# Optimization experiments

Hardware: AMD Instinct MI355X
Metric: run time of the kernel (lower is better)

## Reference

```python
import jax, jax.numpy as jnp
import numpy as np

BETA = 0.5
THR = 1.0
BN_EPS = 1e-5

@jax.custom_vjp
def spike(x):
    # heaviside fire: spk = 1[x > 0]
    return (x > 0).astype(x.dtype)

def _spike_fwd(x):
    return spike(x), x

def _spike_bwd(x, g):
    # snnTorch surrogate.atan(), alpha=2: grad = (alpha/2) / (1 + (pi/2*alpha*x)^2) = 1/(1+(pi*x)^2)
    return (g / (1.0 + (jnp.pi * x) ** 2),)

spike.defvjp(_spike_fwd, _spike_bwd)

def setup_inputs() -> dict:
    key = jax.random.key(0)
    ks = jax.random.split(key, 6)
    B, T, D, O = 512, 128, 512, 10
    data = jax.random.normal(ks[0], (B, T, D), dtype=jnp.float32)
    # deterministic Dropout(0.5) mask in {0, 2} (scaled by 1/keep_prob), time-major
    u = jax.random.uniform(ks[1], (T, B, D), dtype=jnp.float32)
    drop_mask = (u > 0.5).astype(jnp.float32) * 2.0
    W1 = jax.random.normal(ks[2], (D, D), dtype=jnp.float32) / np.sqrt(D)
    b1 = jax.random.normal(ks[3], (D,), dtype=jnp.float32) * 0.01
    gamma = jnp.ones((D,), dtype=jnp.float32)
    bn_beta = jnp.zeros((D,), dtype=jnp.float32)
    W2 = jax.random.normal(ks[4], (O, D), dtype=jnp.float32) / np.sqrt(D)
    b2 = jax.random.normal(ks[5], (O,), dtype=jnp.float32) * 0.01
    return {"data": data, "drop_mask": drop_mask, "W1": W1, "b1": b1,
            "gamma": gamma, "bn_beta": bn_beta, "W2": W2, "b2": b2}

def reference(data, drop_mask, W1, b1, gamma, bn_beta, W2, b2):
    B, T, D = data.shape
    O = W2.shape[0]
    xs = jnp.transpose(data, (1, 0, 2))  # [T, B, D] time-major

    def batchnorm(x):  # training-mode BatchNorm1d over batch dim
        mean = jnp.mean(x, axis=0)
        var = jnp.mean((x - mean) ** 2, axis=0)
        return gamma * (x - mean) * jax.lax.rsqrt(var + BN_EPS) + bn_beta

    def step(carry, inp):
        mem1, spk1, mem2, spk2 = carry
        xt, mt = inp
        cur1 = batchnorm((mt * xt) @ W1.T + b1)          # dropout -> linear -> BN
        mem1 = BETA * mem1 + cur1 - spk1 * THR           # Leaky, subtract reset
        spk1 = spike(mem1 - THR)
        cur2 = spk1 @ W2.T + b2
        mem2 = BETA * mem2 + cur2 - spk2 * THR
        spk2 = spike(mem2 - THR)
        return (mem1, spk1, mem2, spk2), spk2

    init = (jnp.zeros((B, D), data.dtype), jnp.zeros((B, D), data.dtype),
            jnp.zeros((B, O), data.dtype), jnp.zeros((B, O), data.dtype))
    _, spk_rec = jax.lax.scan(step, init, (xs, drop_mask))
    return spk_rec  # [T, B, out_size] == torch.stack(spk_rec)
```

## Files before the change

### kernel.cpp

```cpp
#include <hip/hip_runtime.h>
#include <math.h>

#define B_ 512
#define T_ 128
#define D_ 512
#define O_ 10

typedef unsigned int uint32;
typedef unsigned long long uint64;
typedef short bf16x8 __attribute__((ext_vector_type(8)));
typedef float f32x4 __attribute__((ext_vector_type(4)));

__device__ __forceinline__ uint32 bf16rne(float f) {
    uint32 u = __float_as_uint(f);
    return (u + 0x7FFFu + ((u >> 16) & 1u)) >> 16;
}
__device__ __forceinline__ float bf16f(uint32 h) { return __uint_as_float(h << 16); }

__global__ __launch_bounds__(256)
void presplitW_kernel(const float* __restrict__ W1, unsigned short* __restrict__ Wsp)
{
    const int idx = blockIdx.x * 256 + threadIdx.x;
    const float4 v = *(const float4*)(W1 + (size_t)idx * 4);
    float vv[4] = {v.x, v.y, v.z, v.w};
    uint32 c0[4], c1[4], c2[4];
#pragma unroll
    for (int i = 0; i < 4; ++i) {
        c0[i] = bf16rne(vv[i]);
        float r = vv[i] - bf16f(c0[i]);
        c1[i] = bf16rne(r);
        float r2 = r - bf16f(c1[i]);
        c2[i] = bf16rne(r2);
    }
    const size_t base = (size_t)idx * 4;
    uint2 w;
    w.x = c0[0] | (c0[1] << 16); w.y = c0[2] | (c0[3] << 16);
    *(uint2*)(Wsp + base) = w;
    w.x = c1[0] | (c1[1] << 16); w.y = c1[2] | (c1[3] << 16);
    *(uint2*)(Wsp + 262144 + base) = w;
    w.x = c2[0] | (c2[1] << 16); w.y = c2[2] | (c2[3] << 16);
    *(uint2*)(Wsp + 524288 + base) = w;
}

#define SPW 40
#define SPL (128*SPW)

__global__ __launch_bounds__(256)
void gemm1_kernel(const float* __restrict__ data, const float* __restrict__ drop,
                  const unsigned short* __restrict__ Wsp, const float* __restrict__ b1,
                  float* __restrict__ hbuf, double* __restrict__ pSum,
                  double* __restrict__ pSq, int t0, int Tc)
{
    __shared__ __align__(16) unsigned short As3[3 * SPL];
    __shared__ __align__(16) unsigned short Ws3[3 * SPL];

    const int tid = threadIdx.x;
    const int bid = blockIdx.x;
    const int xcd = bid & 7;
    const int rest = bid >> 3;
    const int yy = rest & 3;
    const int g = (rest >> 2) * 8 + xcd;

    const int R = g * 128;
    const int tc = R >> 9;
    const int b_base = R & 511;
    const int t = t0 + tc;
    const int d0 = yy * 128;

    const int w = tid >> 6;
    const int lane = tid & 63;
    const int wm = w & 1, wn = w >> 1;
    const int q = lane >> 4, r16 = lane & 15;

    f32x4 acc[4][4];
#pragma unroll
    for (int i = 0; i < 4; ++i)
#pragma unroll
        for (int j = 0; j < 4; ++j) acc[i][j] = (f32x4){0.f, 0.f, 0.f, 0.f};

    for (int k0 = 0; k0 < 512; k0 += 32) {
#pragma unroll
        for (int i = 0; i < 2; ++i) {
            const int p = tid + i * 256;
            const int m = p >> 2;
            const int kg = (p & 3) * 8;
            const float* dsrc = data + ((size_t)(b_base + m) * T_ + t) * D_ + k0 + kg;
            const float* msrc = drop + ((size_t)t * B_ + b_base + m) * D_ + k0 + kg;
            const float4 dv0 = *(const float4*)(dsrc);
            const float4 dv1 = *(const float4*)(dsrc + 4);
            const float4 mv0 = *(const float4*)(msrc);
            const float4 mv1 = *(const float4*)(msrc + 4);
            float vv[8] = {dv0.x*mv0.x, dv0.y*mv0.y, dv0.z*mv0.z, dv0.w*mv0.w,
                           dv1.x*mv1.x, dv1.y*mv1.y, dv1.z*mv1.z, dv1.w*mv1.w};
            uint32 u0[8], u1[8], u2[8];
#pragma unroll
            for (int e = 0; e < 8; ++e) {
                u0[e] = bf16rne(vv[e]);
                const float r = vv[e] - bf16f(u0[e]);
                u1[e] = bf16rne(r);
                const float r2 = r - bf16f(u1[e]);
                u2[e] = bf16rne(r2);
            }
            const int dst = m * SPW + kg;
            uint4 pk;
            pk.x = u0[0]|(u0[1]<<16); pk.y = u0[2]|(u0[3]<<16);
            pk.z = u0[4]|(u0[5]<<16); pk.w = u0[6]|(u0[7]<<16);
            *(uint4*)(&As3[dst]) = pk;
            pk.x = u1[0]|(u1[1]<<16); pk.y = u1[2]|(u1[3]<<16);
            pk.z = u1[4]|(u1[5]<<16); pk.w = u1[6]|(u1[7]<<16);
            *(uint4*)(&As3[SPL + dst]) = pk;
            pk.x = u2[0]|(u2[1]<<16); pk.y = u2[2]|(u2[3]<<16);
            pk.z = u2[4]|(u2[5]<<16); pk.w = u2[6]|(u2[7]<<16);
            *(uint4*)(&As3[2*SPL + dst]) = pk;
        }
#pragma unroll
        for (int i = 0; i < 6; ++i) {
            const int p = tid + i * 256;
            const int s = p >> 9;
            const int rem = p & 511;
            const int n = rem >> 2;
            const int kg = (rem & 3) * 8;
            const uint4 pk = *(const uint4*)(Wsp + (size_t)s * 262144
                                             + (size_t)(d0 + n) * 512 + k0 + kg);
            *(uint4*)(&Ws3[s * SPL + n * SPW + kg]) = pk;
        }
        __syncthreads();

        bf16x8 af[4][3], bfr[4][3];
#pragma unroll
        for (int mt = 0; mt < 4; ++mt)
#pragma unroll
            for (int s = 0; s < 3; ++s)
                af[mt][s] = *(const bf16x8*)(&As3[s*SPL + (wm*64 + mt*16 + r16)*SPW + q*8]);
#pragma unroll
        for (int nt = 0; nt < 4; ++nt)
#pragma unroll
            for (int s = 0; s < 3; ++s)
                bfr[nt][s] = *(const bf16x8*)(&Ws3[s*SPL + (wn*64 + nt*16 + r16)*SPW + q*8]);

#define PRODUCT(SA, SB)                                                          \
        {                                                                        \
            _Pragma("unroll")                                                    \
            for (int mt = 0; mt < 4; ++mt) {                                     \
                _Pragma("unroll")                                                \
                for (int nt = 0; nt < 4; ++nt)                                   \
                    acc[mt][nt] = __builtin_amdgcn_mfma_f32_16x16x32_bf16(       \
                        af[mt][SA], bfr[nt][SB], acc[mt][nt], 0, 0, 0);          \
            }                                                                    \
        }
        PRODUCT(0, 0)
        PRODUCT(0, 1)
        PRODUCT(1, 0)
        PRODUCT(1, 1)
        PRODUCT(0, 2)
        PRODUCT(2, 0)
#undef PRODUCT
        __syncthreads();
    }

    float b1c[4];
#pragma unroll
    for (int nt = 0; nt < 4; ++nt) b1c[nt] = b1[d0 + wn*64 + nt*16 + r16];

    double sd[4], sq[4];
#pragma unroll
    for (int nt = 0; nt < 4; ++nt) { sd[nt] = 0.0; sq[nt] = 0.0; }

#pragma unroll
    for (int mt = 0; mt < 4; ++mt)
#pragma unroll
        for (int r = 0; r < 4; ++r) {
            const int row = R + wm*64 + mt*16 + q*4 + r;
            float* op = hbuf + (size_t)row * D_ + d0 + wn*64 + r16;
#pragma unroll
            for (int nt = 0; nt < 4; ++nt) {
                const float hf = acc[mt][nt][r] + b1c[nt];
                op[nt*16] = hf;
                const double dh = (double)hf;
                sd[nt] += dh;
                sq[nt] = fma(dh, dh, sq[nt]);
            }
        }
#pragma unroll
    for (int nt = 0; nt < 4; ++nt) {
        sd[nt] += __shfl_xor(sd[nt], 16); sd[nt] += __shfl_xor(sd[nt], 32);
        sq[nt] += __shfl_xor(sq[nt], 16); sq[nt] += __shfl_xor(sq[nt], 32);
    }
    double* dsh = (double*)&As3[0];
    __syncthreads();
    if (q == 0) {
#pragma unroll
        for (int nt = 0; nt < 4; ++nt) {
            dsh[(w*64 + nt*16 + r16)*2 + 0] = sd[nt];
            dsh[(w*64 + nt*16 + r16)*2 + 1] = sq[nt];
        }
    }
    __syncthreads();
    if (tid < 128) {
        const int col = tid;
        const int gg = col >> 6, c = col & 63;
        const double S = dsh[((2*gg)*64 + c)*2 + 0] + dsh[((2*gg+1)*64 + c)*2 + 0];
        const double Q = dsh[((2*gg)*64 + c)*2 + 1] + dsh[((2*gg+1)*64 + c)*2 + 1];
        const int bt = b_base >> 7;
        pSum[((size_t)(bt*Tc + tc))*D_ + d0 + col] = S;
        pSq [((size_t)(bt*Tc + tc))*D_ + d0 + col] = Q;
    }
}

__global__ __launch_bounds__(256)
void finalize_kernel(const double* __restrict__ pSum, const double* __restrict__ pSq,
                     const float* __restrict__ gamma, const float* __restrict__ bn_beta,
                     float* __restrict__ scaleArr, float* __restrict__ shiftArr, int Tc)
{
    const int tc = blockIdx.x;
    const int d = blockIdx.y * 256 + threadIdx.x;
    double S = 0.0, Q = 0.0;
#pragma unroll
    for (int bt = 0; bt < 4; ++bt) {
        S += pSum[((size_t)(bt * Tc + tc)) * D_ + d];
        Q += pSq [((size_t)(bt * Tc + tc)) * D_ + d];
    }
    const double mean = S / (double)B_;
    const double var  = Q / (double)B_ - mean * mean;
    const double rs   = 1.0 / sqrt(var + 1e-5);
    const double gm   = (double)gamma[d] * rs;
    scaleArr[tc * D_ + d] = (float)gm;
    shiftArr[tc * D_ + d] = (float)((double)bn_beta[d] - gm * mean);
}

__global__ __launch_bounds__(256)
void scanA_kernel(const float* __restrict__ hbuf, const float* __restrict__ scaleArr,
                  const float* __restrict__ shiftArr, uint64* __restrict__ spkM,
                  float* __restrict__ sMem1, float* __restrict__ sSpk1, int t0, int Tc)
{
    const int e = blockIdx.x * 256 + threadIdx.x;
    const int b = e >> 9;
    const int d = e & 511;
    const int lane = threadIdx.x & 63;
    const int mword = (e >> 6);

    float m1, s1;
    if (t0 == 0) { m1 = 0.f; s1 = 0.f; }
    else { m1 = sMem1[e]; s1 = sSpk1[e]; }

    float hv = hbuf[e];
    float sc = scaleArr[d];
    float sf = shiftArr[d];

    for (int tc = 0; tc < Tc; ++tc) {
        float hvN, scN, sfN;
        if (tc + 1 < Tc) {
            hvN = hbuf[(size_t)(tc + 1) * (B_ * D_) + e];
            scN = scaleArr[(tc + 1) * D_ + d];
            sfN = shiftArr[(tc + 1) * D_ + d];
        }
        const float cur1 = fmaf(sc, hv, sf);
        m1 = fmaf(0.5f, m1, cur1) - s1;
        s1 = ((m1 - 1.0f) > 0.f) ? 1.f : 0.f;

        const uint64 mask = __ballot(s1 == 1.f);
        if (lane == 0)
            spkM[(size_t)tc * (B_ * 8) + mword] = mask;

        hv = hvN; sc = scN; sf = sfN;
    }

    sMem1[e] = m1;
    sSpk1[e] = s1;
}

__global__ __launch_bounds__(256)
void gemm2_kernel(const uint64* __restrict__ spkM, const float* __restrict__ W2,
                  const float* __restrict__ b2, float* __restrict__ cur2)
{
    const int tid = threadIdx.x;
    const int w = tid >> 6, lane = tid & 63;
    const int rowBase = blockIdx.x * 16 + w * 4;

    float w2r[O_][8];
#pragma unroll
    for (int o = 0; o < O_; ++o) {
        const float4 wa = *(const float4*)(W2 + o * D_ + lane * 8);
        const float4 wb = *(const float4*)(W2 + o * D_ + lane * 8 + 4);
        w2r[o][0] = wa.x; w2r[o][1] = wa.y; w2r[o][2] = wa.z; w2r[o][3] = wa.w;
        w2r[o][4] = wb.x; w2r[o][5] = wb.y; w2r[o][6] = wb.z; w2r[o][7] = wb.w;
    }
    float b2v[O_];
#pragma unroll
    for (int o = 0; o < O_; ++o) b2v[o] = b2[o];

    for (int rr = 0; rr < 4; ++rr) {
        const int row = rowBase + rr;
        const uint64 mk = spkM[(size_t)row * 8 + (lane >> 3)];
        const uint32 byte = (uint32)(mk >> ((lane & 7) * 8)) & 0xFFu;
        float f[8];
#pragma unroll
        for (int j = 0; j < 8; ++j)
            f[j] = (byte & (1u << j)) ? 1.0f : 0.0f;
        float p[O_];
#pragma unroll
        for (int o = 0; o < O_; ++o) {
            float v = f[0] * w2r[o][0];
#pragma unroll
            for (int j = 1; j < 8; ++j) v = fmaf(f[j], w2r[o][j], v);
            p[o] = v;
        }
#pragma unroll
        for (int o = 0; o < O_; ++o) {
#pragma unroll
            for (int off = 32; off > 0; off >>= 1)
                p[o] += __shfl_xor(p[o], off);
        }
        float outv = 0.f;
#pragma unroll
        for (int o = 0; o < O_; ++o)
            if (lane == o) outv = p[o] + b2v[o];
        if (lane < O_)
            cur2[(size_t)row * O_ + lane] = outv;
    }
}

__global__ __launch_bounds__(256)
void scanB_kernel(const float* __restrict__ cur2, float* __restrict__ out,
                  float* __restrict__ sMem2, float* __restrict__ sSpk2, int t0, int Tc)
{
    const int idx = blockIdx.x * 256 + threadIdx.x;
    float mem2, spk2;
    if (t0 == 0) { mem2 = 0.f; spk2 = 0.f; }
    else { mem2 = sMem2[idx]; spk2 = sSpk2[idx]; }

    float v[4], vn[4];
#pragma unroll
    for (int j = 0; j < 4; ++j) v[j] = cur2[(size_t)j * (B_ * O_) + idx];

    for (int tg = 0; tg < Tc; tg += 4) {
        if (tg + 4 < Tc) {
#pragma unroll
            for (int j = 0; j < 4; ++j)
                vn[j] = cur2[(size_t)(tg + 4 + j) * (B_ * O_) + idx];
        }
#pragma unroll
        for (int j = 0; j < 4; ++j) {
            mem2 = fmaf(0.5f, mem2, v[j]) - spk2;
            spk2 = ((mem2 - 1.0f) > 0.f) ? 1.f : 0.f;
            out[(size_t)(t0 + tg + j) * (B_ * O_) + idx] = spk2;
        }
#pragma unroll
        for (int j = 0; j < 4; ++j) v[j] = vn[j];
    }
    sMem2[idx] = mem2;
    sSpk2[idx] = spk2;
}

extern "C" void kernel_launch(void* const* d_in, const int* in_sizes, int n_in,
                              void* d_out, int out_size, void* d_ws, size_t ws_size,
                              hipStream_t stream) {
    const float* data    = (const float*)d_in[0];
    const float* drop    = (const float*)d_in[1];
    const float* W1      = (const float*)d_in[2];
    const float* b1      = (const float*)d_in[3];
    const float* gamma   = (const float*)d_in[4];
    const float* bn_beta = (const float*)d_in[5];
    const float* W2      = (const float*)d_in[6];
    const float* b2      = (const float*)d_in[7];
    float* out = (float*)d_out;

    const size_t fixedBytes = 1572864 + 2*1048576 + 2*20480;
    const size_t perT = 1048576 + 32768 + 20480 + 4096 + 32768;
    int Tc = T_;
    while (Tc > 2 && fixedBytes + (size_t)Tc * perT > ws_size) Tc >>= 1;

    char* p = (char*)d_ws;
    double* pSum    = (double*)p; p += (size_t)4 * Tc * D_ * 8;
    double* pSq     = (double*)p; p += (size_t)4 * Tc * D_ * 8;
    float* hbuf     = (float*)p; p += (size_t)Tc * B_ * D_ * 4;
    float* scaleArr = (float*)p; p += (size_t)Tc * D_ * 4;
    float* shiftArr = (float*)p; p += (size_t)Tc * D_ * 4;
    float* sMem1    = (float*)p; p += (size_t)B_ * D_ * 4;
    float* sSpk1    = (float*)p; p += (size_t)B_ * D_ * 4;
    float* sMem2    = (float*)p; p += (size_t)B_ * O_ * 4;
    float* sSpk2    = (float*)p; p += (size_t)B_ * O_ * 4;
    float* cur2     = (float*)p; p += (size_t)Tc * B_ * O_ * 4;
    unsigned short* Wsp = (unsigned short*)p; p += (size_t)3 * D_ * D_ * 2;
    uint64* spkM    = (uint64*)p; p += (size_t)Tc * B_ * 8 * 8;

    presplitW_kernel<<<256, 256, 0, stream>>>(W1, Wsp);

    for (int t0 = 0; t0 < T_; t0 += Tc) {
        gemm1_kernel<<<Tc * 16, 256, 0, stream>>>(data, drop, Wsp, b1, hbuf,
                                                  pSum, pSq, t0, Tc);
        finalize_kernel<<<dim3(Tc, D_ / 256), 256, 0, stream>>>(
            pSum, pSq, gamma, bn_beta, scaleArr, shiftArr, Tc);
        scanA_kernel<<<(B_ * D_) / 256, 256, 0, stream>>>(hbuf, scaleArr, shiftArr, spkM,
                                                          sMem1, sSpk1, t0, Tc);
        gemm2_kernel<<<Tc * 32, 256, 0, stream>>>(spkM, W2, b2, cur2);
        scanB_kernel<<<20, 256, 0, stream>>>(cur2, out, sMem2, sSpk2, t0, Tc);
    }
}
```

Measured before the change: 541.0 us.

## Fuse layer-1 scan, output projection and layer-2 scan into one kernel

Replaces the separate scanA, gemm2 and scanB kernels with one kernel that has a block per batch row. Each step, the block builds the spike mask in shared memory, projects it onto W2 and updates the layer-2 membrane in place. This drops the global spkM and cur2 buffers and two launches per chunk. In exchange it adds a __syncthreads per timestep, and every wave redundantly recomputes the full 10-output shuffle reduction for the row.

Measured after the change: 805.2 us. 1.49x slower.

```diff
diff --git a/kernel.cpp b/kernel.cpp
--- a/kernel.cpp
+++ b/kernel.cpp
@@ -228,54 +228,24 @@
     shiftArr[tc * D_ + d] = (float)((double)bn_beta[d] - gm * mean);
 }
 
-__global__ __launch_bounds__(256)
-void scanA_kernel(const float* __restrict__ hbuf, const float* __restrict__ scaleArr,
-                  const float* __restrict__ shiftArr, uint64* __restrict__ spkM,
-                  float* __restrict__ sMem1, float* __restrict__ sSpk1, int t0, int Tc)
+__global__ __launch_bounds__(512)
+void scan_fused_kernel(const float* __restrict__ hbuf, const float* __restrict__ scaleArr,
+                       const float* __restrict__ shiftArr, const float* __restrict__ W2,
+                       const float* __restrict__ b2, float* __restrict__ out,
+                       float* __restrict__ sMem1, float* __restrict__ sSpk1,
+                       float* __restrict__ sMem2, float* __restrict__ sSpk2,
+                       int t0, int Tc)
 {
-    const int e = blockIdx.x * 256 + threadIdx.x;
-    const int b = e >> 9;
-    const int d = e & 511;
-    const int lane = threadIdx.x & 63;
-    const int mword = (e >> 6);
+    const int b = blockIdx.x;
+    const int tid = threadIdx.x;
+    const int w = tid >> 6, lane = tid & 63;
+    const int e = b * D_ + tid;
+
+    __shared__ uint64 masks[2][8];
 
     float m1, s1;
     if (t0 == 0) { m1 = 0.f; s1 = 0.f; }
     else { m1 = sMem1[e]; s1 = sSpk1[e]; }
-
-    float hv = hbuf[e];
-    float sc = scaleArr[d];
-    float sf = shiftArr[d];
-
-    for (int tc = 0; tc < Tc; ++tc) {
-        float hvN, scN, sfN;
-        if (tc + 1 < Tc) {
-            hvN = hbuf[(size_t)(tc + 1) * (B_ * D_) + e];
-            scN = scaleArr[(tc + 1) * D_ + d];
-            sfN = shiftArr[(tc + 1) * D_ + d];
-        }
-        const float cur1 = fmaf(sc, hv, sf);
-        m1 = fmaf(0.5f, m1, cur1) - s1;
-        s1 = ((m1 - 1.0f) > 0.f) ? 1.f : 0.f;
-
-        const uint64 mask = __ballot(s1 == 1.f);
-        if (lane == 0)
-            spkM[(size_t)tc * (B_ * 8) + mword] = mask;
-
-        hv = hvN; sc = scN; sf = sfN;
-    }
-
-    sMem1[e] = m1;
-    sSpk1[e] = s1;
-}
-
-__global__ __launch_bounds__(256)
-void gemm2_kernel(const uint64* __restrict__ spkM, const float* __restrict__ W2,
-                  const float* __restrict__ b2, float* __restrict__ cur2)
-{
-    const int tid = threadIdx.x;
-    const int w = tid >> 6, lane = tid & 63;
-    const int rowBase = blockIdx.x * 16 + w * 4;
 
     float w2r[O_][8];
 #pragma unroll
@@ -289,9 +259,35 @@
 #pragma unroll
     for (int o = 0; o < O_; ++o) b2v[o] = b2[o];
 
-    for (int rr = 0; rr < 4; ++rr) {
-        const int row = rowBase + rr;
-        const uint64 mk = spkM[(size_t)row * 8 + (lane >> 3)];
+    float mem2, spk2;
+    if (t0 == 0) { mem2 = 0.f; spk2 = 0.f; }
+    else {
+        mem2 = (lane < O_) ? sMem2[b * O_ + lane] : 0.f;
+        spk2 = (lane < O_) ? sSpk2[b * O_ + lane] : 0.f;
+    }
+
+    float hv = hbuf[e];
+    float sc = scaleArr[tid];
+    float sf = shiftArr[tid];
+
+    for (int t = 0; t < Tc; ++t) {
+        float hvN, scN, sfN;
+        if (t + 1 < Tc) {
+            hvN = hbuf[(size_t)(t + 1) * (B_ * D_) + e];
+            scN = scaleArr[(t + 1) * D_ + tid];
+            sfN = shiftArr[(t + 1) * D_ + tid];
+        }
+
+        const float cur1 = fmaf(sc, hv, sf);
+        m1 = fmaf(0.5f, m1, cur1) - s1;
+        s1 = ((m1 - 1.0f) > 0.f) ? 1.f : 0.f;
+
+        const uint64 mask = __ballot(s1 == 1.f);
+        const int par = t & 1;
+        if (lane == 0) masks[par][w] = mask;
+        __syncthreads();
+
+        const uint64 mk = masks[par][lane >> 3];
         const uint32 byte = (uint32)(mk >> ((lane & 7) * 8)) & 0xFFu;
         float f[8];
 #pragma unroll
@@ -311,45 +307,27 @@
             for (int off = 32; off > 0; off >>= 1)
                 p[o] += __shfl_xor(p[o], off);
         }
-        float outv = 0.f;
+
+        float c2 = 0.f;
 #pragma unroll
         for (int o = 0; o < O_; ++o)
-            if (lane == o) outv = p[o] + b2v[o];
-        if (lane < O_)
-            cur2[(size_t)row * O_ + lane] = outv;
-    }
-}
-
-__global__ __launch_bounds__(256)
-void scanB_kernel(const float* __restrict__ cur2, float* __restrict__ out,
-                  float* __restrict__ sMem2, float* __restrict__ sSpk2, int t0, int Tc)
-{
-    const int idx = blockIdx.x * 256 + threadIdx.x;
-    float mem2, spk2;
-    if (t0 == 0) { mem2 = 0.f; spk2 = 0.f; }
-    else { mem2 = sMem2[idx]; spk2 = sSpk2[idx]; }
-
-    float v[4], vn[4];
-#pragma unroll
-    for (int j = 0; j < 4; ++j) v[j] = cur2[(size_t)j * (B_ * O_) + idx];
-
-    for (int tg = 0; tg < Tc; tg += 4) {
-        if (tg + 4 < Tc) {
-#pragma unroll
-            for (int j = 0; j < 4; ++j)
-                vn[j] = cur2[(size_t)(tg + 4 + j) * (B_ * O_) + idx];
-        }
-#pragma unroll
-        for (int j = 0; j < 4; ++j) {
-            mem2 = fmaf(0.5f, mem2, v[j]) - spk2;
+            if (lane == o) c2 = p[o] + b2v[o];
+        if (lane < O_) {
+            mem2 = fmaf(0.5f, mem2, c2) - spk2;
             spk2 = ((mem2 - 1.0f) > 0.f) ? 1.f : 0.f;
-            out[(size_t)(t0 + tg + j) * (B_ * O_) + idx] = spk2;
-        }
-#pragma unroll
-        for (int j = 0; j < 4; ++j) v[j] = vn[j];
-    }
-    sMem2[idx] = mem2;
-    sSpk2[idx] = spk2;
+            if (w == 0)
+                out[(size_t)(t0 + t) * (B_ * O_) + b * O_ + lane] = spk2;
+        }
+
+        hv = hvN; sc = scN; sf = sfN;
+    }
+
+    sMem1[e] = m1;
+    sSpk1[e] = s1;
+    if (w == 0 && lane < O_) {
+        sMem2[b * O_ + lane] = mem2;
+        sSpk2[b * O_ + lane] = spk2;
+    }
 }
 
 extern "C" void kernel_launch(void* const* d_in, const int* in_sizes, int n_in,
@@ -365,8 +343,8 @@
     const float* b2      = (const float*)d_in[7];
     float* out = (float*)d_out;
 
-    const size_t fixedBytes = 1572864 + 2*1048576 + 2*20480;
-    const size_t perT = 1048576 + 32768 + 20480 + 4096 + 32768;
+    const size_t fixedBytes = 1572864  + 2*1048576  + 2*20480;
+    const size_t perT = 1048576 + 4096 + 32768;
     int Tc = T_;
     while (Tc > 2 && fixedBytes + (size_t)Tc * perT > ws_size) Tc >>= 1;
 
@@ -380,9 +358,7 @@
     float* sSpk1    = (float*)p; p += (size_t)B_ * D_ * 4;
     float* sMem2    = (float*)p; p += (size_t)B_ * O_ * 4;
     float* sSpk2    = (float*)p; p += (size_t)B_ * O_ * 4;
-    float* cur2     = (float*)p; p += (size_t)Tc * B_ * O_ * 4;
     unsigned short* Wsp = (unsigned short*)p; p += (size_t)3 * D_ * D_ * 2;
-    uint64* spkM    = (uint64*)p; p += (size_t)Tc * B_ * 8 * 8;
 
     presplitW_kernel<<<256, 256, 0, stream>>>(W1, Wsp);
 
@@ -391,9 +367,7 @@
                                                   pSum, pSq, t0, Tc);
         finalize_kernel<<<dim3(Tc, D_ / 256), 256, 0, stream>>>(
             pSum, pSq, gamma, bn_beta, scaleArr, shiftArr, Tc);
-        scanA_kernel<<<(B_ * D_) / 256, 256, 0, stream>>>(hbuf, scaleArr, shiftArr, spkM,
-                                                          sMem1, sSpk1, t0, Tc);
-        gemm2_kernel<<<Tc * 32, 256, 0, stream>>>(spkM, W2, b2, cur2);
-        scanB_kernel<<<20, 256, 0, stream>>>(cur2, out, sMem2, sSpk2, t0, Tc);
-    }
-}
+        scan_fused_kernel<<<B_, 512, 0, stream>>>(hbuf, scaleArr, shiftArr, W2, b2, out,
+                                                  sMem1, sSpk1, sMem2, sSpk2, t0, Tc);
+    }
+}
```
